# Performance work log

Measured on AMD Instinct MI355X. Metric: run time of the kernel, lower is better.

Reference implementation:

```python
import jax, jax.numpy as jnp
import numpy as np

EPS = 1e-5


def _rln(x, w, b, m1w, m1b, m2w, m2b):
    # Revised LayerNorm (DehazeFormer): per-sample stats over (C,H,W)
    mean = jnp.mean(x, axis=(1, 2, 3), keepdims=True)            # [b,1,1,1]
    std = jnp.sqrt(jnp.mean((x - mean) ** 2, axis=(1, 2, 3), keepdims=True) + EPS)
    normed = (x - mean) / std * w + b                            # [b,C,H,W]
    rescale = std * m1w + m1b                                    # 1x1 conv from 1 channel
    rebias = mean * m2w + m2b
    return normed, rescale, rebias


def _pconv(x, W, b):
    # 1x1 conv as channel contraction: W [out,in], x [b,in,h,w]
    return jnp.einsum('oi,bihw->bohw', W, x) + b[None, :, None, None]


def setup_inputs() -> dict:
    key = jax.random.key(0)
    ks = jax.random.split(key, 24)
    B, C, H, W = 8, 96, 128, 128
    p = lambda k, shp, s=0.02: (jax.random.normal(k, shp, dtype=jnp.float32) * s)
    inp = {
        'x_u': jax.random.normal(ks[0], (B, C, H, W), dtype=jnp.float32),
        'x_d': jax.random.normal(ks[1], (B, C, H, W), dtype=jnp.float32),
        # RLN (u)
        'nw_u': jnp.ones((1, C, 1, 1), jnp.float32),
        'nb_u': jnp.zeros((1, C, 1, 1), jnp.float32),
        'm1w_u': p(ks[2], (1, C, 1, 1)), 'm1b_u': p(ks[3], (1, C, 1, 1)),
        'm2w_u': p(ks[4], (1, C, 1, 1)), 'm2b_u': p(ks[5], (1, C, 1, 1)),
        # RLN (d)
        'nw_d': jnp.ones((1, C, 1, 1), jnp.float32),
        'nb_d': jnp.zeros((1, C, 1, 1), jnp.float32),
        'm1w_d': p(ks[6], (1, C, 1, 1)), 'm1b_d': p(ks[7], (1, C, 1, 1)),
        'm2w_d': p(ks[8], (1, C, 1, 1)), 'm2b_d': p(ks[9], (1, C, 1, 1)),
        # 1x1 qkv convs
        'Wqkv_u': p(ks[10], (2 * C, C)), 'bqkv_u': jnp.zeros((2 * C,), jnp.float32),
        'Wqkv_d': p(ks[11], (2 * C, C)), 'bqkv_d': jnp.zeros((2 * C,), jnp.float32),
        # learned scalar scales
        'scale_h': jnp.ones((1,), jnp.float32),
        'scale_w': jnp.ones((1,), jnp.float32),
        'scale_c': jnp.ones((1,), jnp.float32),
    }
    return inp


def reference(x_u, x_d,
              nw_u, nb_u, m1w_u, m1b_u, m2w_u, m2b_u,
              nw_d, nb_d, m1w_d, m1b_d, m2w_d, m2b_d,
              Wqkv_u, bqkv_u, Wqkv_d, bqkv_d,
              scale_h, scale_w, scale_c):
    x_d_norm, resc_d, bias_d = _rln(x_d, nw_d, nb_d, m1w_d, m1b_d, m2w_d, m2b_d)
    x_u_norm, resc_u, bias_u = _rln(x_u, nw_u, nb_u, m1w_u, m1b_u, m2w_u, m2b_u)

    q_u, v_u = jnp.split(_pconv(x_u_norm, Wqkv_u, bqkv_u), 2, axis=1)
    k_d, v_d = jnp.split(_pconv(x_d_norm, Wqkv_d, bqkv_d), 2, axis=1)

    q_h, q_w, q_c = jnp.split(q_u, 3, axis=1)
    k_h, k_w, k_c = jnp.split(k_d, 3, axis=1)
    vu_h, vu_w, vu_c = jnp.split(v_u, 3, axis=1)
    vd_h, vd_w, vd_c = jnp.split(v_d, 3, axis=1)

    # ---- height-axis attention: per (b,w), scores over h x h ----
    A_h = jax.nn.softmax(jnp.einsum('bciw,bcjw->bwij', q_h, k_h) * scale_h[0], axis=-1)
    d2u_h = jnp.einsum('bwij,bcjw->bciw', A_h, vd_h)            # attn @ v_d
    u2d_h = jnp.einsum('bwij,bciw->bcjw', A_h, vu_h)            # attn^T @ v_u

    # ---- width-axis attention: per (b,h), scores over w x w ----
    S_w = jnp.einsum('bchi,bchj->bhij', q_w, k_w) * scale_w[0]
    d2u_w = jnp.einsum('bhij,bchj->bchi', jax.nn.softmax(S_w, axis=-1), vd_w)
    # softmax(S_w^T, -1) @ v_u  ==  softmax over axis -2, contracted over i
    u2d_w = jnp.einsum('bhij,bchi->bchj', jax.nn.softmax(S_w, axis=-2), vu_w)

    # ---- channel-axis attention: per b, scores over c x c ----
    b, c, h, w = q_c.shape
    qc = q_c.reshape(b, c, h * w)
    kc = k_c.reshape(b, c, h * w)
    A_c = jax.nn.softmax(jnp.einsum('bcn,bdn->bcd', qc, kc) * scale_c[0], axis=-1)
    d2u_c = jnp.einsum('bcd,bdn->bcn', A_c, vd_c.reshape(b, c, h * w)).reshape(b, c, h, w)
    # NOTE: original code uses the same (non-transposed) softmax for u2d_c
    u2d_c = jnp.einsum('bcd,bdn->bcn', A_c, vu_c.reshape(b, c, h * w)).reshape(b, c, h, w)

    x_d2u = jnp.concatenate([d2u_h, d2u_w, d2u_c], axis=1)
    x_u2d = jnp.concatenate([u2d_h, u2d_w, u2d_c], axis=1)

    out_u = x_d2u * resc_u + bias_u + x_u
    out_d = x_u2d * resc_d + bias_d + x_d
    return out_u + out_d
```

## Files before the change

kernel.cpp:

```cpp
#include <hip/hip_runtime.h>
#include <math.h>

#define NB 8
#define NC 96
#define NH 128
#define NWID 128
#define NN (NH*NWID)
#define NCO 192
#define NM (NC*NN)

#define WS_SUMS   0
#define WS_SC     32
#define WS_AC     8224
#define WS_SU     16416
#define WS_TU     17184
#define WS_SD     17952
#define WS_TD     18720
#define WS_RU     19488
#define WS_RD     20256
#define WS_CADD   21024
#define WS_BPU    21792
#define WS_BPD    23328
#define WS_WB16   24864
#define WS_QKV16  327680
#define QKV16_D   25165824ull
#define WS_SLABS  25493504
#define SLAB_SZ   4194304ull
#define OFF_QH    (0*SLAB_SZ)
#define OFF_KH    (1*SLAB_SZ)
#define OFF_QW    (2*SLAB_SZ)
#define OFF_KW    (3*SLAB_SZ)
#define OFF_VHU   (4*SLAB_SZ)
#define OFF_VHD   (5*SLAB_SZ)
#define OFF_VWU   (6*SLAB_SZ)
#define OFF_VWD   (7*SLAB_SZ)
#define WS_OH     44892160

typedef __attribute__((ext_vector_type(8))) short bf16x8;
typedef __attribute__((ext_vector_type(4))) float f32x4;

static __device__ __forceinline__ float bf2f(ushort u){ return __uint_as_float(((uint)u) << 16); }
static __device__ __forceinline__ ushort f2bf(float f){
  uint b = __float_as_uint(f);
  return (ushort)((b + 0x7fffu + ((b >> 16) & 1u)) >> 16);
}
static __device__ __forceinline__ bf16x8 ldfrag(const ushort* p){
  union { uint4 u; bf16x8 b; } cv; cv.u = *(const uint4*)p; return cv.b;
}

__global__ __launch_bounds__(256) void reduce_stats(const float* __restrict__ xu,
                                                    const float* __restrict__ xd,
                                                    float* __restrict__ ws) {
  int blk = blockIdx.x;
  int tensor = blk >> 9;
  int b = (blk >> 6) & 7;
  int chunk = blk & 63;
  const float* x = tensor ? xd : xu;
  const float4* p = (const float4*)(x + (size_t)b*NM + (size_t)chunk*(NM/64));
  float s = 0.f, sq = 0.f;
  for (int r = 0; r < 24; r++) {
    float4 v = p[threadIdx.x + r*256];
    s  += v.x + v.y + v.z + v.w;
    sq += v.x*v.x + v.y*v.y + v.z*v.z + v.w*v.w;
  }
  for (int o = 32; o; o >>= 1) { s += __shfl_down(s, o); sq += __shfl_down(sq, o); }
  __shared__ float ls[8];
  int wv = threadIdx.x >> 6, ln = threadIdx.x & 63;
  if (ln == 0) { ls[wv*2] = s; ls[wv*2+1] = sq; }
  __syncthreads();
  if (threadIdx.x == 0) {
    s  = ls[0] + ls[2] + ls[4] + ls[6];
    sq = ls[1] + ls[3] + ls[5] + ls[7];
    atomicAdd(&ws[WS_SUMS + (tensor*8 + b)*2],     s);
    atomicAdd(&ws[WS_SUMS + (tensor*8 + b)*2 + 1], sq);
  }
}

__global__ void compute_params(float* __restrict__ ws,
    const float* __restrict__ nwu, const float* __restrict__ nbu,
    const float* __restrict__ m1wu, const float* __restrict__ m1bu,
    const float* __restrict__ m2wu, const float* __restrict__ m2bu,
    const float* __restrict__ nwd, const float* __restrict__ nbd,
    const float* __restrict__ m1wd, const float* __restrict__ m1bd,
    const float* __restrict__ m2wd, const float* __restrict__ m2bd,
    const float* __restrict__ Wqu, const float* __restrict__ bqu,
    const float* __restrict__ Wqd, const float* __restrict__ bqd) {
  __shared__ float meanL[16], stdL[16];
  __shared__ float tuL[768], tdL[768];
  int t = threadIdx.x;
  if (t < 16) {
    float s = ws[WS_SUMS + t*2], sq = ws[WS_SUMS + t*2 + 1];
    const float inv = 1.f / (float)NM;
    float mean = s * inv;
    float var  = sq * inv - mean*mean;
    meanL[t] = mean;
    stdL[t]  = sqrtf(var + 1e-5f);
  }
  __syncthreads();
  for (int idx = t; idx < 768; idx += 256) {
    int b = idx / 96, c = idx % 96;
    float mu = meanL[b],   su = stdL[b];
    float md = meanL[8+b], sd = stdL[8+b];
    float scu = nwu[c] / su;
    float scd = nwd[c] / sd;
    float tcu = nbu[c] - mu*scu;
    float tcd = nbd[c] - md*scd;
    tuL[idx] = tcu; tdL[idx] = tcd;
    ws[WS_SU+idx] = scu; ws[WS_TU+idx] = tcu;
    ws[WS_SD+idx] = scd; ws[WS_TD+idx] = tcd;
    ws[WS_RU+idx] = su*m1wu[c] + m1bu[c];
    ws[WS_RD+idx] = sd*m1wd[c] + m1bd[c];
    ws[WS_CADD+idx] = (mu*m2wu[c] + m2bu[c]) + (md*m2wd[c] + m2bd[c]);
  }
  __syncthreads();
  for (int idx = t; idx < 3072; idx += 256) {
    int tensor = idx / 1536;
    int r = idx % 1536;
    int b = r / 192, o = r % 192;
    const float* Wq = tensor ? Wqd : Wqu;
    const float* tt = tensor ? tdL : tuL;
    float acc = tensor ? bqd[o] : bqu[o];
    for (int i = 0; i < 96; i++) acc += Wq[o*96 + i] * tt[b*96 + i];
    ws[(tensor ? WS_BPD : WS_BPU) + r] = acc;
  }
}

__global__ __launch_bounds__(256) void compute_wprime(float* __restrict__ ws,
    const float* __restrict__ Wqu, const float* __restrict__ Wqd) {
  int idx = blockIdx.x*256 + threadIdx.x;
  if (idx >= 319488) return;
  int tensor = idx / 159744;
  int r = idx % 159744;
  int b  = r / 19968;
  int r2 = r % 19968;
  int o  = r2 / 104, i = r2 % 104;
  ushort* wb = (ushort*)(ws + WS_WB16);
  ushort v = 0;
  if (i < 96) {
    const float* Wq = tensor ? Wqd : Wqu;
    const float* s  = ws + (tensor ? WS_SD : WS_SU);
    v = f2bf(Wq[o*96 + i] * s[b*96 + i]);
  }
  wb[idx] = v;
}

__global__ __launch_bounds__(256) void qkv_gemm(float* __restrict__ ws,
    const float* __restrict__ xu, const float* __restrict__ xd) {
  __shared__ __align__(16) ushort QL[16640];
  ushort* Bl = QL;
  ushort* Ah = QL + 6656;
  int blk = blockIdx.x;
  int tensor = blk >> 11;
  int rem = blk & 2047;
  int b = rem >> 8;
  int r2 = rem & 255;
  int nt = r2 >> 1;
  int wh = r2 & 1;
  int n0 = nt*128 + wh*64;
  const float* x = (tensor ? xd : xu) + (size_t)b*NM;
  const ushort* wb = (const ushort*)(ws + WS_WB16) + (size_t)(tensor*8 + b)*19968;
  const float* bp = ws + (tensor ? WS_BPD : WS_BPU) + b*192;
  ushort* outq16 = (ushort*)(ws + WS_QKV16) + (tensor ? QKV16_D : 0) + (size_t)b*NCO*NN;
  ushort* slab = (ushort*)(ws + WS_SLABS);
  const int t = threadIdx.x;
  const int wv = t >> 6, lid = t & 63, l15 = lid & 15, l4 = lid >> 4;

  for (int it = 0; it < 3; it++) {
    int idx = t + it*256;
    int i2 = (idx & 7) | ((idx >> 7) << 3);
    int n4 = (idx >> 3) & 15;
    const float* r0 = x + (size_t)(2*i2)*NN + n0 + n4*4;
    float4 a0 = *(const float4*)r0;
    float4 a1 = *(const float4*)(r0 + NN);
    uint p0 = (uint)f2bf(a0.x) | ((uint)f2bf(a1.x) << 16);
    uint p1 = (uint)f2bf(a0.y) | ((uint)f2bf(a1.y) << 16);
    uint p2 = (uint)f2bf(a0.z) | ((uint)f2bf(a1.z) << 16);
    uint p3 = (uint)f2bf(a0.w) | ((uint)f2bf(a1.w) << 16);
    ushort* base = &Bl[(size_t)(n4*4)*104 + 2*i2];
    *(uint*)(base)           = p0;
    *(uint*)(base + 104)     = p1;
    *(uint*)(base + 208)     = p2;
    *(uint*)(base + 312)     = p3;
  }
  for (int it = 0; it < 5; it++) {
    int idx = t + it*256;
    if (idx < 1248) ((uint4*)Ah)[idx] = ((const uint4*)wb)[idx];
  }
  __syncthreads();

  bf16x8 bfr[3];
  #pragma unroll
  for (int s = 0; s < 3; s++)
    bfr[s] = ldfrag(&Bl[(wv*16 + l15)*104 + s*32 + l4*8]);

  f32x4 z4 = {0.f,0.f,0.f,0.f};
  f32x4 acc[12];
  #pragma unroll
  for (int mt = 0; mt < 12; mt++) acc[mt] = z4;
  #pragma unroll
  for (int s = 0; s < 3; s++) {
    #pragma unroll
    for (int mt = 0; mt < 6; mt++) {
      bf16x8 a = ldfrag(&Ah[(mt*16 + l15)*104 + s*32 + l4*8]);
      acc[mt] = __builtin_amdgcn_mfma_f32_16x16x32_bf16(a, bfr[s], acc[mt], 0, 0, 0);
    }
  }
  __syncthreads();
  for (int it = 0; it < 5; it++) {
    int idx = t + it*256;
    if (idx < 1248) ((uint4*)Ah)[idx] = ((const uint4*)wb)[1248 + idx];
  }
  __syncthreads();
  #pragma unroll
  for (int s = 0; s < 3; s++) {
    #pragma unroll
    for (int mt = 0; mt < 6; mt++) {
      bf16x8 a = ldfrag(&Ah[(mt*16 + l15)*104 + s*32 + l4*8]);
      acc[6+mt] = __builtin_amdgcn_mfma_f32_16x16x32_bf16(a, bfr[s], acc[6+mt], 0, 0, 0);
    }
  }
  __syncthreads();
  ushort* Cl = QL;
  #pragma unroll
  for (int mt = 0; mt < 12; mt++) {
    #pragma unroll
    for (int r = 0; r < 4; r++) {
      int o = mt*16 + l4*4 + r;
      Cl[o*72 + wv*16 + l15] = f2bf(acc[mt][r] + bp[o]);
    }
  }
  __syncthreads();
  for (int it = 0; it < 3; it++) {
    int idx = t + it*256;
    int lr = idx >> 3, ch = idx & 7;
    int o = (lr < 64) ? (64 + lr) : (96 + lr);
    *(uint4*)(outq16 + (size_t)o*NN + n0 + ch*8) = *(const uint4*)&Cl[o*72 + ch*8];
  }
  if (t < 128) {
    int axis = t >> 6, w = t & 63;
    ushort* dstq = slab + (tensor ? (axis ? OFF_KW : OFF_KH) : (axis ? OFF_QW : OFF_QH));
    size_t o = axis ? ((size_t)(b*128 + nt)*128 + wh*64 + w)*32
                    : ((size_t)(b*128 + wh*64 + w)*128 + nt)*32;
    uint uu[16];
    #pragma unroll
    for (int k = 0; k < 16; k++) {
      ushort a0 = Cl[(axis*32 + 2*k)*72 + w];
      ushort a1 = Cl[(axis*32 + 2*k + 1)*72 + w];
      uu[k] = (uint)a0 | ((uint)a1 << 16);
    }
    *(uint4*)(dstq + o)      = make_uint4(uu[0],uu[1],uu[2],uu[3]);
    *(uint4*)(dstq + o + 8)  = make_uint4(uu[4],uu[5],uu[6],uu[7]);
    *(uint4*)(dstq + o + 16) = make_uint4(uu[8],uu[9],uu[10],uu[11]);
    *(uint4*)(dstq + o + 24) = make_uint4(uu[12],uu[13],uu[14],uu[15]);
  }
  {
    ushort* dstv = slab + (tensor ? OFF_VWD : OFF_VWU);
    int c = t >> 3, ch = t & 7;
    *(uint4*)(dstv + ((size_t)(b*128 + nt)*32 + c)*128 + wh*64 + ch*8) =
        *(const uint4*)&Cl[(128 + c)*72 + ch*8];
  }
}

__global__ __launch_bounds__(256) void qkv_prep(float* __restrict__ ws) {
  __shared__ __align__(16) ushort Br[16*1320];
  int bid = blockIdx.x;
  int tensor = bid >> 8;
  int r = bid & 255;
  int cb = r >> 7, b = (r >> 4) & 7, hb = (r >> 2) & 3, wb = r & 3;
  const ushort* qkv16 = (const ushort*)(ws + WS_QKV16);
  const ushort* src = qkv16 + (tensor ? QKV16_D : 0)
                    + (size_t)b*NCO*NN + (size_t)(96 + cb*16)*NN;
  ushort* dst = (ushort*)(ws + WS_SLABS) + (tensor ? OFF_VHD : OFF_VHU);
  int t = threadIdx.x;
  for (int k = 0; k < 8; k++) {
    int idx = t + k*256;
    int c = idx >> 7, h = (idx >> 2) & 31, w8 = idx & 3;
    uint4 v = *(const uint4*)(src + (size_t)c*NN + (size_t)(hb*32 + h)*NWID + wb*32 + w8*8);
    *(uint4*)&Br[c*1320 + h*40 + w8*8] = v;
  }
  __syncthreads();
  for (int k = 0; k < 2; k++) {
    int idx = t + k*256;
    int w = idx >> 4, c = idx & 15;
    uint uu[16];
    #pragma unroll
    for (int hh = 0; hh < 16; hh++) {
      ushort a0 = Br[c*1320 + (2*hh)*40 + w];
      ushort a1 = Br[c*1320 + (2*hh+1)*40 + w];
      uu[hh] = (uint)a0 | ((uint)a1 << 16);
    }
    size_t o = ((size_t)(b*128 + wb*32 + w)*32 + cb*16 + c)*128 + hb*32;
    *(uint4*)(dst + o)      = make_uint4(uu[0],uu[1],uu[2],uu[3]);
    *(uint4*)(dst + o + 8)  = make_uint4(uu[4],uu[5],uu[6],uu[7]);
    *(uint4*)(dst + o + 16) = make_uint4(uu[8],uu[9],uu[10],uu[11]);
    *(uint4*)(dst + o + 24) = make_uint4(uu[12],uu[13],uu[14],uu[15]);
  }
}

__global__ __launch_bounds__(256) void attn_both(float* __restrict__ ws,
    const float* __restrict__ xu, const float* __restrict__ xd,
    float* __restrict__ out, const float* __restrict__ sch, const float* __restrict__ scw) {
  __shared__ __align__(16) ushort SMEM[36352];
  __shared__ float m1s[128], l1s[128];
  const int t = threadIdx.x;

  if (blockIdx.x >= 2048) {
    float* qs = (float*)SMEM;
    float* ks = qs + 8320;
    int bid = blockIdx.x - 2048;
    int b = bid >> 6, chunk = bid & 63;
    int n0 = chunk * 256;
    const ushort* qkv16 = (const ushort*)(ws + WS_QKV16);
    const ushort* qp = qkv16 + ((size_t)b*NCO + 64)*NN + n0;
    const ushort* kp = qkv16 + QKV16_D + ((size_t)b*NCO + 64)*NN + n0;
    for (int r = 0; r < 4; r++) {
      int idx = t + r*256;
      int c = idx >> 5, n8 = idx & 31;
      uint4 v = *(const uint4*)(qp + (size_t)c*NN + n8*8);
      uint4 w = *(const uint4*)(kp + (size_t)c*NN + n8*8);
      float* q  = &qs[c*260 + n8*8];
      float* kk = &ks[c*260 + n8*8];
      q[0] = bf2f((ushort)(v.x & 0xffff)); q[1] = bf2f((ushort)(v.x >> 16));
      q[2] = bf2f((ushort)(v.y & 0xffff)); q[3] = bf2f((ushort)(v.y >> 16));
      q[4] = bf2f((ushort)(v.z & 0xffff)); q[5] = bf2f((ushort)(v.z >> 16));
      q[6] = bf2f((ushort)(v.w & 0xffff)); q[7] = bf2f((ushort)(v.w >> 16));
      kk[0] = bf2f((ushort)(w.x & 0xffff)); kk[1] = bf2f((ushort)(w.x >> 16));
      kk[2] = bf2f((ushort)(w.y & 0xffff)); kk[3] = bf2f((ushort)(w.y >> 16));
      kk[4] = bf2f((ushort)(w.z & 0xffff)); kk[5] = bf2f((ushort)(w.z >> 16));
      kk[6] = bf2f((ushort)(w.w & 0xffff)); kk[7] = bf2f((ushort)(w.w >> 16));
    }
    __syncthreads();
    int d = t & 31, cbq = t >> 5;
    float a[4] = {0.f,0.f,0.f,0.f};
    for (int n4 = 0; n4 < 64; n4++) {
      float4 kv = *(const float4*)&ks[d*260 + n4*4];
      #pragma unroll
      for (int r = 0; r < 4; r++) {
        float4 qv = *(const float4*)&qs[(cbq + 8*r)*260 + n4*4];
        a[r] += qv.x*kv.x + qv.y*kv.y + qv.z*kv.z + qv.w*kv.w;
      }
    }
    #pragma unroll
    for (int r = 0; r < 4; r++)
      atomicAdd(&ws[WS_SC + b*1024 + (cbq + 8*r)*32 + d], a[r]);
    return;
  }

  ushort* Qs  = SMEM;
  ushort* Ks  = SMEM + 5120;
  ushort* Vds = SMEM + 10240;
  ushort* Vus = SMEM + 14592;
  ushort* Pl  = SMEM + 18944;
  const int AXIS = blockIdx.x >> 10;
  const int rem = blockIdx.x & 1023;
  const int b = rem >> 7, p2 = rem & 127;
  const int wv = t >> 6, lid = t & 63, l15 = lid & 15, l4 = lid >> 4;
  const ushort* slab = (const ushort*)(ws + WS_SLABS);
  const ushort* qsrc  = slab + (AXIS ? OFF_QW : OFF_QH) + (size_t)(b*128 + p2)*4096;
  const ushort* ksrc  = slab + (AXIS ? OFF_KW : OFF_KH) + (size_t)(b*128 + p2)*4096;
  const ushort* vdsrc = slab + (AXIS ? OFF_VWD : OFF_VHD) + (size_t)(b*128 + p2)*4096;
  const ushort* vusrc = slab + (AXIS ? OFF_VWU : OFF_VHU) + (size_t)(b*128 + p2)*4096;
  for (int i = t; i < 2048; i += 256) {
    if (i < 512) {
      int row = i >> 2, q = i & 3;
      *(uint4*)&Qs[row*40 + q*8] = *(const uint4*)(qsrc + row*32 + q*8);
    } else if (i < 1024) {
      int j = i - 512, row = j >> 2, q = j & 3;
      *(uint4*)&Ks[row*40 + q*8] = *(const uint4*)(ksrc + row*32 + q*8);
    } else if (i < 1536) {
      int j = i - 1024, row = j >> 4, ch = j & 15;
      *(uint4*)&Vds[row*136 + ch*8] = *(const uint4*)(vdsrc + row*128 + ch*8);
    } else {
      int j = i - 1536, row = j >> 4, ch = j & 15;
      *(uint4*)&Vus[row*136 + ch*8] = *(const uint4*)(vusrc + row*128 + ch*8);
    }
  }
  const float sc = (AXIS ? scw : sch)[0];
  const int cbas = AXIS ? 32 : 0;
  float ruv0 = ws[WS_RU + b*96 + cbas + l15];
  float ruv1 = ws[WS_RU + b*96 + cbas + 16 + l15];
  float rdv0 = ws[WS_RD + b*96 + cbas + l15];
  float rdv1 = ws[WS_RD + b*96 + cbas + 16 + l15];
  __syncthreads();

  f32x4 z4 = {0.f,0.f,0.f,0.f};
  f32x4 s1[2][8];
  {
    bf16x8 bfr[8];
    #pragma unroll
    for (int tj = 0; tj < 8; tj++) bfr[tj] = ldfrag(&Ks[(tj*16 + l15)*40 + l4*8]);
    #pragma unroll
    for (int ti = 0; ti < 2; ti++) {
      bf16x8 a = ldfrag(&Qs[((2*wv+ti)*16 + l15)*40 + l4*8]);
      #pragma unroll
      for (int tj = 0; tj < 8; tj++)
        s1[ti][tj] = __builtin_amdgcn_mfma_f32_16x16x32_bf16(a, bfr[tj], z4, 0, 0, 0);
    }
  }
  #pragma unroll
  for (int ti = 0; ti < 2; ti++) {
    #pragma unroll
    for (int r = 0; r < 4; r++) {
      float mx = -3.0e38f;
      #pragma unroll
      for (int tj = 0; tj < 8; tj++) { float v = s1[ti][tj][r]*sc; s1[ti][tj][r] = v; mx = fmaxf(mx, v); }
      mx = fmaxf(mx, __shfl_xor(mx, 1)); mx = fmaxf(mx, __shfl_xor(mx, 2));
      mx = fmaxf(mx, __shfl_xor(mx, 4)); mx = fmaxf(mx, __shfl_xor(mx, 8));
      float sm = 0.f;
      #pragma unroll
      for (int tj = 0; tj < 8; tj++) { float e = __expf(s1[ti][tj][r] - mx); s1[ti][tj][r] = e; sm += e; }
      sm += __shfl_xor(sm, 1); sm += __shfl_xor(sm, 2); sm += __shfl_xor(sm, 4); sm += __shfl_xor(sm, 8);
      int row = 32*wv + ti*16 + l4*4 + r;
      if (l15 == 0) { m1s[row] = mx; l1s[row] = sm; }
      float inv = __fdividef(1.f, sm);
      #pragma unroll
      for (int tj = 0; tj < 8; tj++) Pl[row*136 + tj*16 + l15] = f2bf(s1[ti][tj][r]*inv);
    }
  }
  __syncthreads();
  f32x4 o1[2][2] = {{z4,z4},{z4,z4}};
  #pragma unroll
  for (int ks = 0; ks < 4; ks++) {
    bf16x8 bv0 = ldfrag(&Vds[l15*136 + ks*32 + l4*8]);
    bf16x8 bv1 = ldfrag(&Vds[(16 + l15)*136 + ks*32 + l4*8]);
    #pragma unroll
    for (int mt = 0; mt < 2; mt++) {
      bf16x8 a = ldfrag(&Pl[((2*wv+mt)*16 + l15)*136 + ks*32 + l4*8]);
      o1[mt][0] = __builtin_amdgcn_mfma_f32_16x16x32_bf16(a, bv0, o1[mt][0], 0, 0, 0);
      o1[mt][1] = __builtin_amdgcn_mfma_f32_16x16x32_bf16(a, bv1, o1[mt][1], 0, 0, 0);
    }
  }
  {
    bf16x8 bq[8];
    #pragma unroll
    for (int it = 0; it < 8; it++) bq[it] = ldfrag(&Qs[(it*16 + l15)*40 + l4*8]);
    #pragma unroll
    for (int tjt = 0; tjt < 2; tjt++) {
      bf16x8 a = ldfrag(&Ks[((2*wv+tjt)*16 + l15)*40 + l4*8]);
      #pragma unroll
      for (int it = 0; it < 8; it++)
        s1[tjt][it] = __builtin_amdgcn_mfma_f32_16x16x32_bf16(a, bq[it], z4, 0, 0, 0);
    }
  }
  if (AXIS == 1) {
    #pragma unroll
    for (int tjt = 0; tjt < 2; tjt++) {
      #pragma unroll
      for (int r = 0; r < 4; r++) {
        float mx = -3.0e38f;
        #pragma unroll
        for (int it = 0; it < 8; it++) { float v = s1[tjt][it][r]*sc; s1[tjt][it][r] = v; mx = fmaxf(mx, v); }
        mx = fmaxf(mx, __shfl_xor(mx, 1)); mx = fmaxf(mx, __shfl_xor(mx, 2));
        mx = fmaxf(mx, __shfl_xor(mx, 4)); mx = fmaxf(mx, __shfl_xor(mx, 8));
        float sm = 0.f;
        #pragma unroll
        for (int it = 0; it < 8; it++) { float e = __expf(s1[tjt][it][r] - mx); s1[tjt][it][r] = e; sm += e; }
        sm += __shfl_xor(sm, 1); sm += __shfl_xor(sm, 2); sm += __shfl_xor(sm, 4); sm += __shfl_xor(sm, 8);
        float inv = __fdividef(1.f, sm);
        #pragma unroll
        for (int it = 0; it < 8; it++) s1[tjt][it][r] *= inv;
      }
    }
  } else {
    float mi[8], li[8];
    #pragma unroll
    for (int it = 0; it < 8; it++) {
      mi[it] = m1s[it*16 + l15];
      li[it] = __fdividef(1.f, l1s[it*16 + l15]);
    }
    #pragma unroll
    for (int tjt = 0; tjt < 2; tjt++)
      #pragma unroll
      for (int it = 0; it < 8; it++)
        #pragma unroll
        for (int r = 0; r < 4; r++)
          s1[tjt][it][r] = __expf(s1[tjt][it][r]*sc - mi[it]) * li[it];
  }
  __syncthreads();
  #pragma unroll
  for (int tjt = 0; tjt < 2; tjt++)
    #pragma unroll
    for (int r = 0; r < 4; r++) {
      int row = 32*wv + tjt*16 + l4*4 + r;
      #pragma unroll
      for (int it = 0; it < 8; it++) Pl[row*136 + it*16 + l15] = f2bf(s1[tjt][it][r]);
    }
  __syncthreads();
  f32x4 o2[2][2] = {{z4,z4},{z4,z4}};
  #pragma unroll
  for (int ks = 0; ks < 4; ks++) {
    bf16x8 bv0 = ldfrag(&Vus[l15*136 + ks*32 + l4*8]);
    bf16x8 bv1 = ldfrag(&Vus[(16 + l15)*136 + ks*32 + l4*8]);
    #pragma unroll
    for (int mt = 0; mt < 2; mt++) {
      bf16x8 a = ldfrag(&Pl[((2*wv+mt)*16 + l15)*136 + ks*32 + l4*8]);
      o2[mt][0] = __builtin_amdgcn_mfma_f32_16x16x32_bf16(a, bv0, o2[mt][0], 0, 0, 0);
      o2[mt][1] = __builtin_amdgcn_mfma_f32_16x16x32_bf16(a, bv1, o2[mt][1], 0, 0, 0);
    }
  }
  __syncthreads();
  float* St = (float*)Pl;
  #pragma unroll
  for (int mt = 0; mt < 2; mt++)
    #pragma unroll
    for (int nt = 0; nt < 2; nt++) {
      float ru = nt ? ruv1 : ruv0;
      float rd = nt ? rdv1 : rdv0;
      float4 vv;
      vv.x = o1[mt][nt][0]*ru + o2[mt][nt][0]*rd;
      vv.y = o1[mt][nt][1]*ru + o2[mt][nt][1]*rd;
      vv.z = o1[mt][nt][2]*ru + o2[mt][nt][2]*rd;
      vv.w = o1[mt][nt][3]*ru + o2[mt][nt][3]*rd;
      *(float4*)&St[(nt*16 + l15)*132 + (2*wv+mt)*16 + l4*4] = vv;
    }
  __syncthreads();
  if (AXIS == 1) {
    for (int k = 0; k < 4; k++) {
      int idx = t + k*256;
      int c = idx >> 5, p4 = idx & 31;
      float4 v = *(const float4*)&St[c*132 + p4*4];
      float ca = ws[WS_CADD + b*96 + 32 + c];
      size_t off = ((size_t)(b*NC + 32 + c)*NH + p2)*NWID + p4*4;
      float4 a = *(const float4*)(xu + off);
      float4 dd = *(const float4*)(xd + off);
      v.x += ca + a.x + dd.x; v.y += ca + a.y + dd.y;
      v.z += ca + a.z + dd.z; v.w += ca + a.w + dd.w;
      *(float4*)(out + off) = v;
    }
  } else {
    ushort* oh16 = (ushort*)(ws + WS_OH);
    for (int k = 0; k < 2; k++) {
      int idx = t + k*256;
      int c = idx >> 4, p8 = idx & 15;
      const float* src = &St[c*132 + p8*8];
      uint4 pk;
      pk.x = (uint)f2bf(src[0]) | ((uint)f2bf(src[1]) << 16);
      pk.y = (uint)f2bf(src[2]) | ((uint)f2bf(src[3]) << 16);
      pk.z = (uint)f2bf(src[4]) | ((uint)f2bf(src[5]) << 16);
      pk.w = (uint)f2bf(src[6]) | ((uint)f2bf(src[7]) << 16);
      *(uint4*)(oh16 + ((size_t)(b*128 + p2)*32 + c)*128 + p8*8) = pk;
    }
  }
}

__global__ __launch_bounds__(256) void merge_h(float* __restrict__ ws,
    const float* __restrict__ xu, const float* __restrict__ xd,
    float* __restrict__ out) {
  __shared__ float T[32][33];
  int bid = blockIdx.x;
  int b = bid >> 9, c = (bid >> 4) & 31, ht = (bid >> 2) & 3, wt = bid & 3;
  int t = threadIdx.x;
  const ushort* oh16 = (const ushort*)(ws + WS_OH);
  {
    int w = t >> 3, hq = t & 7;
    uint2 v = *(const uint2*)(oh16 + ((size_t)(b*128 + wt*32 + w)*32 + c)*128 + ht*32 + hq*4);
    T[w][hq*4+0] = bf2f((ushort)(v.x & 0xffff));
    T[w][hq*4+1] = bf2f((ushort)(v.x >> 16));
    T[w][hq*4+2] = bf2f((ushort)(v.y & 0xffff));
    T[w][hq*4+3] = bf2f((ushort)(v.y >> 16));
  }
  __syncthreads();
  {
    int h = t >> 3, w4 = t & 7;
    float ca = ws[WS_CADD + b*96 + c];
    size_t off = ((size_t)(b*NC + c)*NH + ht*32 + h)*NWID + wt*32 + w4*4;
    float4 a = *(const float4*)(xu + off);
    float4 d = *(const float4*)(xd + off);
    float4 v;
    v.x = T[w4*4+0][h] + ca + a.x + d.x;
    v.y = T[w4*4+1][h] + ca + a.y + d.y;
    v.z = T[w4*4+2][h] + ca + a.z + d.z;
    v.w = T[w4*4+3][h] + ca + a.w + d.w;
    *(float4*)(out + off) = v;
  }
}

__global__ void attn_c2(float* __restrict__ ws, const float* __restrict__ scale_p) {
  int b = blockIdx.x, c = threadIdx.x;
  if (c >= 32) return;
  float sc = scale_p[0];
  float row[32];
  float m = -3.0e38f;
  for (int d = 0; d < 32; d++) { row[d] = ws[WS_SC + b*1024 + c*32 + d] * sc; m = fmaxf(m, row[d]); }
  float s = 0.f;
  for (int d = 0; d < 32; d++) { row[d] = __expf(row[d] - m); s += row[d]; }
  float inv = 1.f / s;
  for (int d = 0; d < 32; d++) ws[WS_AC + b*1024 + c*32 + d] = row[d]*inv;
}

__global__ __launch_bounds__(256) void attn_c3(float* __restrict__ ws,
    const float* __restrict__ xu, const float* __restrict__ xd,
    float* __restrict__ out) {
  __shared__ float AsT[32][36];
  __shared__ float ruL[32], rdL[32], caL[32];
  int b = blockIdx.x >> 6, chunk = blockIdx.x & 63;
  int t = threadIdx.x;
  for (int r = 0; r < 4; r++) {
    int idx = t + r*256;
    int c = idx >> 5, d = idx & 31;
    AsT[d][c] = ws[WS_AC + b*1024 + idx];
  }
  if (t < 32) {
    ruL[t] = ws[WS_RU + b*96 + 64 + t];
    rdL[t] = ws[WS_RD + b*96 + 64 + t];
    caL[t] = ws[WS_CADD + b*96 + 64 + t];
  }
  __syncthreads();
  int n = chunk*256 + t;
  const ushort* qkv16 = (const ushort*)(ws + WS_QKV16);
  const ushort* vdp = qkv16 + QKV16_D + ((size_t)b*NCO + 160)*NN + n;
  const ushort* vup = qkv16 + ((size_t)b*NCO + 160)*NN + n;
  float acc1[32], acc2[32];
  #pragma unroll
  for (int c2 = 0; c2 < 32; c2++) { acc1[c2]=0.f; acc2[c2]=0.f; }
  for (int d = 0; d < 32; d++) {
    float vd = bf2f(vdp[(size_t)d*NN]);
    float vu = bf2f(vup[(size_t)d*NN]);
    #pragma unroll
    for (int c4 = 0; c4 < 8; c4++) {
      float4 av = *(const float4*)&AsT[d][c4*4];
      acc1[c4*4+0] += av.x*vd; acc2[c4*4+0] += av.x*vu;
      acc1[c4*4+1] += av.y*vd; acc2[c4*4+1] += av.y*vu;
      acc1[c4*4+2] += av.z*vd; acc2[c4*4+2] += av.z*vu;
      acc1[c4*4+3] += av.w*vd; acc2[c4*4+3] += av.w*vu;
    }
  }
  size_t base = ((size_t)(b*NC) + 64)*NN + n;
  #pragma unroll
  for (int c2 = 0; c2 < 32; c2++) {
    size_t off = base + (size_t)c2*NN;
    out[off] = acc1[c2]*ruL[c2] + acc2[c2]*rdL[c2] + caL[c2] + xu[off] + xd[off];
  }
}

extern "C" void kernel_launch(void* const* d_in, const int* in_sizes, int n_in,
                              void* d_out, int out_size, void* d_ws, size_t ws_size,
                              hipStream_t stream) {
  (void)in_sizes; (void)n_in; (void)out_size; (void)ws_size;
  const float* xu   = (const float*)d_in[0];
  const float* xd   = (const float*)d_in[1];
  const float* nwu  = (const float*)d_in[2];
  const float* nbu  = (const float*)d_in[3];
  const float* m1wu = (const float*)d_in[4];
  const float* m1bu = (const float*)d_in[5];
  const float* m2wu = (const float*)d_in[6];
  const float* m2bu = (const float*)d_in[7];
  const float* nwd  = (const float*)d_in[8];
  const float* nbd  = (const float*)d_in[9];
  const float* m1wd = (const float*)d_in[10];
  const float* m1bd = (const float*)d_in[11];
  const float* m2wd = (const float*)d_in[12];
  const float* m2bd = (const float*)d_in[13];
  const float* Wqu  = (const float*)d_in[14];
  const float* bqu  = (const float*)d_in[15];
  const float* Wqd  = (const float*)d_in[16];
  const float* bqd  = (const float*)d_in[17];
  const float* sch  = (const float*)d_in[18];
  const float* scw  = (const float*)d_in[19];
  const float* scc  = (const float*)d_in[20];
  float* ws  = (float*)d_ws;
  float* out = (float*)d_out;

  hipMemsetAsync(d_ws, 0, 8224*sizeof(float), stream);
  reduce_stats<<<1024, 256, 0, stream>>>(xu, xd, ws);
  compute_params<<<1, 256, 0, stream>>>(ws, nwu, nbu, m1wu, m1bu, m2wu, m2bu,
                                        nwd, nbd, m1wd, m1bd, m2wd, m2bd,
                                        Wqu, bqu, Wqd, bqd);
  compute_wprime<<<1248, 256, 0, stream>>>(ws, Wqu, Wqd);
  qkv_gemm<<<4096, 256, 0, stream>>>(ws, xu, xd);
  qkv_prep<<<512, 256, 0, stream>>>(ws);
  attn_both<<<2560, 256, 0, stream>>>(ws, xu, xd, out, sch, scw);
  merge_h<<<4096, 256, 0, stream>>>(ws, xu, xd, out);
  attn_c2<<<8, 64, 0, stream>>>(ws, scc);
  attn_c3<<<512, 256, 0, stream>>>(ws, xu, xd, out);
}
```

Measured before the change: 237.8 us.

## Use MFMA for channel score partials and fuse channel softmax into attn_c3

The channel-attention score blocks in attn_both now keep q/k tiles in LDS as bf16 and compute the 32x32 partial scores with bf16 MFMA instructions, instead of converting to fp32 and doing scalar dot products. This removes the conversion work and most of the LDS traffic. The separate attn_c2 softmax kernel is removed, and each attn_c3 block recomputes the 32x32 softmax from the raw scores in shared memory, saving one kernel launch. The trade-off is redundant softmax work in every attn_c3 block and an extra barrier.

```diff
diff --git a/kernel.cpp b/kernel.cpp
--- a/kernel.cpp
+++ b/kernel.cpp
@@ -305,44 +305,40 @@
   const int t = threadIdx.x;
 
   if (blockIdx.x >= 2048) {
-    float* qs = (float*)SMEM;
-    float* ks = qs + 8320;
+    ushort* qs16 = SMEM;
+    ushort* ks16 = SMEM + 8448;
     int bid = blockIdx.x - 2048;
     int b = bid >> 6, chunk = bid & 63;
     int n0 = chunk * 256;
     const ushort* qkv16 = (const ushort*)(ws + WS_QKV16);
     const ushort* qp = qkv16 + ((size_t)b*NCO + 64)*NN + n0;
     const ushort* kp = qkv16 + QKV16_D + ((size_t)b*NCO + 64)*NN + n0;
+    for (int it = 0; it < 8; it++) {
+      int idx = t + it*256;
+      int mat = idx >> 10;
+      int r = idx & 1023;
+      int c = r >> 5, n8 = r & 31;
+      const ushort* src = (mat ? kp : qp) + (size_t)c*NN + n8*8;
+      ushort* dst = (mat ? ks16 : qs16) + c*264 + n8*8;
+      *(uint4*)dst = *(const uint4*)src;
+    }
+    __syncthreads();
+    const int wv = t >> 6, lid = t & 63, l15 = lid & 15, l4 = lid >> 4;
+    const int cr = wv >> 1, dc = wv & 1;
+    f32x4 z4 = {0.f,0.f,0.f,0.f};
+    f32x4 acc = z4;
+    #pragma unroll
+    for (int ks = 0; ks < 8; ks++) {
+      bf16x8 a = ldfrag(&qs16[(cr*16 + l15)*264 + ks*32 + l4*8]);
+      bf16x8 bq = ldfrag(&ks16[(dc*16 + l15)*264 + ks*32 + l4*8]);
+      acc = __builtin_amdgcn_mfma_f32_16x16x32_bf16(a, bq, acc, 0, 0, 0);
+    }
+    #pragma unroll
     for (int r = 0; r < 4; r++) {
-      int idx = t + r*256;
-      int c = idx >> 5, n8 = idx & 31;
-      uint4 v = *(const uint4*)(qp + (size_t)c*NN + n8*8);
-      uint4 w = *(const uint4*)(kp + (size_t)c*NN + n8*8);
-      float* q  = &qs[c*260 + n8*8];
-      float* kk = &ks[c*260 + n8*8];
-      q[0] = bf2f((ushort)(v.x & 0xffff)); q[1] = bf2f((ushort)(v.x >> 16));
-      q[2] = bf2f((ushort)(v.y & 0xffff)); q[3] = bf2f((ushort)(v.y >> 16));
-      q[4] = bf2f((ushort)(v.z & 0xffff)); q[5] = bf2f((ushort)(v.z >> 16));
-      q[6] = bf2f((ushort)(v.w & 0xffff)); q[7] = bf2f((ushort)(v.w >> 16));
-      kk[0] = bf2f((ushort)(w.x & 0xffff)); kk[1] = bf2f((ushort)(w.x >> 16));
-      kk[2] = bf2f((ushort)(w.y & 0xffff)); kk[3] = bf2f((ushort)(w.y >> 16));
-      kk[4] = bf2f((ushort)(w.z & 0xffff)); kk[5] = bf2f((ushort)(w.z >> 16));
-      kk[6] = bf2f((ushort)(w.w & 0xffff)); kk[7] = bf2f((ushort)(w.w >> 16));
-    }
-    __syncthreads();
-    int d = t & 31, cbq = t >> 5;
-    float a[4] = {0.f,0.f,0.f,0.f};
-    for (int n4 = 0; n4 < 64; n4++) {
-      float4 kv = *(const float4*)&ks[d*260 + n4*4];
-      #pragma unroll
-      for (int r = 0; r < 4; r++) {
-        float4 qv = *(const float4*)&qs[(cbq + 8*r)*260 + n4*4];
-        a[r] += qv.x*kv.x + qv.y*kv.y + qv.z*kv.z + qv.w*kv.w;
-      }
-    }
-    #pragma unroll
-    for (int r = 0; r < 4; r++)
-      atomicAdd(&ws[WS_SC + b*1024 + (cbq + 8*r)*32 + d], a[r]);
+      int c = cr*16 + l4*4 + r;
+      int d = dc*16 + l15;
+      atomicAdd(&ws[WS_SC + b*1024 + c*32 + d], acc[r]);
+    }
     return;
   }
 
@@ -575,22 +571,10 @@
   }
 }
 
-__global__ void attn_c2(float* __restrict__ ws, const float* __restrict__ scale_p) {
-  int b = blockIdx.x, c = threadIdx.x;
-  if (c >= 32) return;
-  float sc = scale_p[0];
-  float row[32];
-  float m = -3.0e38f;
-  for (int d = 0; d < 32; d++) { row[d] = ws[WS_SC + b*1024 + c*32 + d] * sc; m = fmaxf(m, row[d]); }
-  float s = 0.f;
-  for (int d = 0; d < 32; d++) { row[d] = __expf(row[d] - m); s += row[d]; }
-  float inv = 1.f / s;
-  for (int d = 0; d < 32; d++) ws[WS_AC + b*1024 + c*32 + d] = row[d]*inv;
-}
-
 __global__ __launch_bounds__(256) void attn_c3(float* __restrict__ ws,
     const float* __restrict__ xu, const float* __restrict__ xd,
-    float* __restrict__ out) {
+    float* __restrict__ out, const float* __restrict__ scale_p) {
+  __shared__ float scl[32][33];
   __shared__ float AsT[32][36];
   __shared__ float ruL[32], rdL[32], caL[32];
   int b = blockIdx.x >> 6, chunk = blockIdx.x & 63;
@@ -598,12 +582,23 @@
   for (int r = 0; r < 4; r++) {
     int idx = t + r*256;
     int c = idx >> 5, d = idx & 31;
-    AsT[d][c] = ws[WS_AC + b*1024 + idx];
+    scl[c][d] = ws[WS_SC + b*1024 + idx];
   }
   if (t < 32) {
     ruL[t] = ws[WS_RU + b*96 + 64 + t];
     rdL[t] = ws[WS_RD + b*96 + 64 + t];
     caL[t] = ws[WS_CADD + b*96 + 64 + t];
+  }
+  __syncthreads();
+  if (t < 32) {
+    float sc = scale_p[0];
+    float row[32];
+    float m = -3.0e38f;
+    for (int d = 0; d < 32; d++) { row[d] = scl[t][d] * sc; m = fmaxf(m, row[d]); }
+    float s = 0.f;
+    for (int d = 0; d < 32; d++) { row[d] = __expf(row[d] - m); s += row[d]; }
+    float inv = 1.f / s;
+    for (int d = 0; d < 32; d++) AsT[d][t] = row[d]*inv;
   }
   __syncthreads();
   int n = chunk*256 + t;
@@ -671,6 +666,5 @@
   qkv_prep<<<512, 256, 0, stream>>>(ws);
   attn_both<<<2560, 256, 0, stream>>>(ws, xu, xd, out, sch, scw);
   merge_h<<<4096, 256, 0, stream>>>(ws, xu, xd, out);
-  attn_c2<<<8, 64, 0, stream>>>(ws, scc);
-  attn_c3<<<512, 256, 0, stream>>>(ws, xu, xd, out);
-}
+  attn_c3<<<512, 256, 0, stream>>>(ws, xu, xd, out, scc);
+}
```

Result: faster. 232.1 us (-2.4%).
